# Kernel tuning notes

Hardware: AMD Instinct MI355X
Metric: run time of the kernel (lower is better)

## Reference

```python
import jax, jax.numpy as jnp
import numpy as np

N = 32767      # 2**15 - 1 nodes: complete binary tree, parent(i) = (i-1)//2
IN = 512       # in_channels
H = 256        # hidden_dim
OUT = 1        # output_dim
DEPTH = 15     # number of topological levels (static)


def setup_inputs() -> dict:
    key = jax.random.key(0)
    ks = jax.random.split(key, 8)
    x = jax.random.normal(ks[0], (N, IN), dtype=jnp.float32)
    # complete binary tree edge list: edge_index[0]=child, edge_index[1]=parent
    src = jnp.arange(1, N, dtype=jnp.int32)
    dst = (src - 1) // 2
    edge_index = jnp.stack([src, dst])  # [2, N-1]
    s = 1.0 / np.sqrt(H)  # torch LSTMCell/Linear default uniform init scale
    W_ih = jax.random.uniform(ks[1], (4 * H, IN), minval=-s, maxval=s, dtype=jnp.float32)
    W_hh = jax.random.uniform(ks[2], (4 * H, H), minval=-s, maxval=s, dtype=jnp.float32)
    b_ih = jax.random.uniform(ks[3], (4 * H,), minval=-s, maxval=s, dtype=jnp.float32)
    b_hh = jax.random.uniform(ks[4], (4 * H,), minval=-s, maxval=s, dtype=jnp.float32)
    W_fc = jax.random.uniform(ks[5], (OUT, H), minval=-s, maxval=s, dtype=jnp.float32)
    b_fc = jax.random.uniform(ks[6], (OUT,), minval=-s, maxval=s, dtype=jnp.float32)
    return {"x": x, "edge_index": edge_index, "W_ih": W_ih, "W_hh": W_hh,
            "b_ih": b_ih, "b_hh": b_hh, "W_fc": W_fc, "b_fc": b_fc}


def reference(x, edge_index, W_ih, W_hh, b_ih, b_hh, W_fc, b_fc):
    src, dst = edge_index[0], edge_index[1]
    # children count per parent (matches torch children_count loop)
    cnt = jax.ops.segment_sum(jnp.ones_like(src, dtype=x.dtype), dst, num_segments=N)
    cnt = jnp.maximum(cnt, 1.0)[:, None]  # [N,1]; leaves get zero child state anyway
    h = jnp.zeros((N, H), dtype=x.dtype)
    c = jnp.zeros((N, H), dtype=x.dtype)
    # topological sweep: deepest level first (children processed before parents)
    for d in range(DEPTH - 1, -1, -1):
        lo = 2 ** d - 1
        hi = min(2 ** (d + 1) - 1, N)  # level d node index range (static)
        # mean of already-computed child h/c states, gathered via edge list
        mean_h = jax.ops.segment_sum(h[src], dst, num_segments=N)[lo:hi] / cnt[lo:hi]
        mean_c = jax.ops.segment_sum(c[src], dst, num_segments=N)[lo:hi] / cnt[lo:hi]
        # torch LSTMCell: gates in (i, f, g, o) order
        gates = x[lo:hi] @ W_ih.T + b_ih + mean_h @ W_hh.T + b_hh  # [n_level, 4H]
        i, f, g, o = jnp.split(gates, 4, axis=-1)
        i, f, o = jax.nn.sigmoid(i), jax.nn.sigmoid(f), jax.nn.sigmoid(o)
        g = jnp.tanh(g)
        c_new = f * mean_c + i * g
        h_new = o * jnp.tanh(c_new)
        h = h.at[lo:hi].set(h_new)
        c = c.at[lo:hi].set(c_new)
    pooled = jnp.mean(h, axis=0, keepdims=True)  # [1, H]
    out = pooled @ W_fc.T + b_fc                 # [1, 1]
    return out.squeeze(-1)                       # [1]
```

## Files before the change

kernel.cpp:

```cpp
#include <hip/hip_runtime.h>
#include <math.h>


#define N_NODES 32767
#define N_LEAF0 16383
#define IN_C    512
#define H_C     256

typedef __bf16 bf16x8 __attribute__((ext_vector_type(8)));
typedef float  f32x4  __attribute__((ext_vector_type(4)));

__device__ __forceinline__ void gload_lds16(const void* g, void* l) {
    __builtin_amdgcn_global_load_lds(
        (const __attribute__((address_space(1))) unsigned int*)g,
        (__attribute__((address_space(3))) unsigned int*)l,
        16, 0, 0);
}

__device__ __forceinline__ float fast_rcp(float x) { return __builtin_amdgcn_rcpf(x); }
__device__ __forceinline__ float sigm(float x)     { return fast_rcp(1.f + __expf(-x)); }
__device__ __forceinline__ float tanh_fast(float x){ return 2.f * fast_rcp(1.f + __expf(-2.f * x)) - 1.f; }

__global__ __launch_bounds__(256)
void conv_bf16_kernel(const float* __restrict__ src, __bf16* __restrict__ dst, int n8)
{
    const int i = blockIdx.x * 256 + threadIdx.x;
    if (i < n8) {
        const float4* s4 = (const float4*)src;
        const float4 a = s4[2 * i];
        const float4 b = s4[2 * i + 1];
        bf16x8 o;
        o[0] = (__bf16)a.x; o[1] = (__bf16)a.y; o[2] = (__bf16)a.z; o[3] = (__bf16)a.w;
        o[4] = (__bf16)b.x; o[5] = (__bf16)b.y; o[6] = (__bf16)b.z; o[7] = (__bf16)b.w;
        *(bf16x8*)(dst + 8 * i) = o;
    }
}

__global__ __launch_bounds__(256)
void bulk_xw(const float* __restrict__ x,
             const __bf16* __restrict__ wih,
             const float* __restrict__ b_ih,
             const float* __restrict__ b_hh,
             __bf16* __restrict__ hb,
             float* __restrict__ c,
             __bf16* __restrict__ gx)
{
    __shared__ __bf16 As[128 * 32];
    __shared__ __bf16 Bs[128 * 32];

    const int t    = threadIdx.x;
    const int lane = t & 63;
    const int wv   = t >> 6;
    const int wm   = wv >> 1;
    const int wn   = wv & 1;
    const int quad = lane >> 4;
    const int l15  = lane & 15;
    const int cb   = blockIdx.x;
    const int m0   = blockIdx.y * 128;

    f32x4 acc[4][4];
#pragma unroll
    for (int mi = 0; mi < 4; ++mi)
#pragma unroll
        for (int ni = 0; ni < 4; ++ni) acc[mi][ni] = (f32x4)0.f;

    for (int k0 = 0; k0 < IN_C; k0 += 32) {
#pragma unroll
        for (int e = 0; e < 2; ++e) {
            const int chunk = wv * 2 + e;
            const int nl    = chunk * 16 + (lane >> 2);
            const int q     = (nl >> 4) & 3;
            const int cc    = (nl & 15) + ((nl >> 6) << 4);
            const int grow  = q * H_C + cb * 32 + cc;
            const void* g = (const char*)(wih + grow * IN_C + k0) + (lane & 3) * 16;
            gload_lds16(g, (char*)Bs + chunk * 1024);
        }
        {
            const int row  = t >> 1;
            const int kh   = (t & 1) * 16;
            const int node = min(m0 + row, N_NODES - 1);
            const float4* xs = (const float4*)(x + (size_t)node * IN_C + k0 + kh);
            const float4 v0 = xs[0], v1 = xs[1], v2 = xs[2], v3 = xs[3];
            bf16x8 o0, o1;
            o0[0] = (__bf16)v0.x; o0[1] = (__bf16)v0.y; o0[2] = (__bf16)v0.z; o0[3] = (__bf16)v0.w;
            o0[4] = (__bf16)v1.x; o0[5] = (__bf16)v1.y; o0[6] = (__bf16)v1.z; o0[7] = (__bf16)v1.w;
            o1[0] = (__bf16)v2.x; o1[1] = (__bf16)v2.y; o1[2] = (__bf16)v2.z; o1[3] = (__bf16)v2.w;
            o1[4] = (__bf16)v3.x; o1[5] = (__bf16)v3.y; o1[6] = (__bf16)v3.z; o1[7] = (__bf16)v3.w;
            bf16x8* dst = (bf16x8*)(As + row * 32 + kh);
            dst[0] = o0;
            dst[1] = o1;
        }
        __syncthreads();
        bf16x8 af[4], bfr[4];
#pragma unroll
        for (int mi = 0; mi < 4; ++mi)
            af[mi] = *(const bf16x8*)(As + (wm * 64 + mi * 16 + l15) * 32 + quad * 8);
#pragma unroll
        for (int ni = 0; ni < 4; ++ni)
            bfr[ni] = *(const bf16x8*)(Bs + (wn * 64 + ni * 16 + l15) * 32 + quad * 8);
#pragma unroll
        for (int mi = 0; mi < 4; ++mi)
#pragma unroll
            for (int ni = 0; ni < 4; ++ni)
                acc[mi][ni] = __builtin_amdgcn_mfma_f32_16x16x32_bf16(
                    af[mi], bfr[ni], acc[mi][ni], 0, 0, 0);
        __syncthreads();
    }

    const int CH = cb * 32 + wn * 16 + l15;
    float bs[4];
#pragma unroll
    for (int q = 0; q < 4; ++q) bs[q] = b_ih[q * H_C + CH] + b_hh[q * H_C + CH];

#pragma unroll
    for (int mi = 0; mi < 4; ++mi) {
#pragma unroll
        for (int r = 0; r < 4; ++r) {
            const int m = m0 + wm * 64 + mi * 16 + quad * 4 + r;
            if (m >= N_NODES) continue;
            if (m >= N_LEAF0) {
                const float gi = sigm(acc[mi][0][r] + bs[0]);
                const float gf = sigm(acc[mi][1][r] + bs[1]);  (void)gf;
                const float gg = tanh_fast(acc[mi][2][r] + bs[2]);
                const float go = sigm(acc[mi][3][r] + bs[3]);
                const float cn = gi * gg;
                const float hn = go * tanh_fast(cn);
                c[(size_t)m * H_C + CH] = cn;
                hb[(size_t)m * H_C + CH] = (__bf16)hn;
            } else {
#pragma unroll
                for (int q = 0; q < 4; ++q)
                    gx[(size_t)m * 1024 + q * H_C + CH] = (__bf16)acc[mi][q][r];
            }
        }
    }
}

__global__ __launch_bounds__(256)
void level_hw(const __bf16* __restrict__ whh,
              const float* __restrict__ b_ih,
              const float* __restrict__ b_hh,
              const __bf16* __restrict__ gx,
              __bf16* __restrict__ hb,
              float* __restrict__ c,
              int lo, int n)
{
    __shared__ __bf16 As[128 * 32];
    __shared__ __bf16 Bs[128 * 32];

    const int t    = threadIdx.x;
    const int lane = t & 63;
    const int wv   = t >> 6;
    const int wm   = wv >> 1;
    const int wn   = wv & 1;
    const int quad = lane >> 4;
    const int l15  = lane & 15;
    const int cb   = blockIdx.x;
    const int m0   = blockIdx.y * 128;

    f32x4 acc[4][4];
#pragma unroll
    for (int mi = 0; mi < 4; ++mi)
#pragma unroll
        for (int ni = 0; ni < 4; ++ni) acc[mi][ni] = (f32x4)0.f;

    for (int k0 = 0; k0 < H_C; k0 += 32) {
#pragma unroll
        for (int e = 0; e < 2; ++e) {
            const int chunk = wv * 2 + e;
            const int nl    = chunk * 16 + (lane >> 2);
            const int q     = (nl >> 4) & 3;
            const int cc    = (nl & 15) + ((nl >> 6) << 4);
            const int grow  = q * H_C + cb * 32 + cc;
            const void* g = (const char*)(whh + grow * H_C + k0) + (lane & 3) * 16;
            gload_lds16(g, (char*)Bs + chunk * 1024);
        }
        {
            const int row  = t >> 1;
            const int kh   = (t & 1) * 16;
            const int node = lo + m0 + row;
            const int k2   = k0 + kh;
            const bf16x8* hl = (const bf16x8*)(hb + (size_t)(2 * node + 1) * H_C + k2);
            const bf16x8* hr = (const bf16x8*)(hb + (size_t)(2 * node + 2) * H_C + k2);
            const bf16x8 a0 = hl[0], a1 = hl[1], b0 = hr[0], b1 = hr[1];
            bf16x8 o0, o1;
#pragma unroll
            for (int j = 0; j < 8; ++j) {
                o0[j] = (__bf16)(0.5f * ((float)a0[j] + (float)b0[j]));
                o1[j] = (__bf16)(0.5f * ((float)a1[j] + (float)b1[j]));
            }
            bf16x8* dst = (bf16x8*)(As + row * 32 + kh);
            dst[0] = o0;
            dst[1] = o1;
        }
        __syncthreads();
        bf16x8 af[4], bfr[4];
#pragma unroll
        for (int mi = 0; mi < 4; ++mi)
            af[mi] = *(const bf16x8*)(As + (wm * 64 + mi * 16 + l15) * 32 + quad * 8);
#pragma unroll
        for (int ni = 0; ni < 4; ++ni)
            bfr[ni] = *(const bf16x8*)(Bs + (wn * 64 + ni * 16 + l15) * 32 + quad * 8);
#pragma unroll
        for (int mi = 0; mi < 4; ++mi)
#pragma unroll
            for (int ni = 0; ni < 4; ++ni)
                acc[mi][ni] = __builtin_amdgcn_mfma_f32_16x16x32_bf16(
                    af[mi], bfr[ni], acc[mi][ni], 0, 0, 0);
        __syncthreads();
    }

    const int CH = cb * 32 + wn * 16 + l15;
    float bs[4];
#pragma unroll
    for (int q = 0; q < 4; ++q) bs[q] = b_ih[q * H_C + CH] + b_hh[q * H_C + CH];

#pragma unroll
    for (int mi = 0; mi < 4; ++mi) {
#pragma unroll
        for (int r = 0; r < 4; ++r) {
            const int m = m0 + wm * 64 + mi * 16 + quad * 4 + r;
            if (m < n) {
                const int node = lo + m;
                const float g0 = acc[mi][0][r] + (float)gx[(size_t)node * 1024 + 0 * H_C + CH] + bs[0];
                const float g1 = acc[mi][1][r] + (float)gx[(size_t)node * 1024 + 1 * H_C + CH] + bs[1];
                const float g2 = acc[mi][2][r] + (float)gx[(size_t)node * 1024 + 2 * H_C + CH] + bs[2];
                const float g3 = acc[mi][3][r] + (float)gx[(size_t)node * 1024 + 3 * H_C + CH] + bs[3];
                const float gi = sigm(g0);
                const float gf = sigm(g1);
                const float gg = tanh_fast(g2);
                const float go = sigm(g3);
                const float mc = 0.5f * (c[(size_t)(2 * node + 1) * H_C + CH] +
                                         c[(size_t)(2 * node + 2) * H_C + CH]);
                const float cn = gf * mc + gi * gg;
                const float hn = go * tanh_fast(cn);
                c[(size_t)node * H_C + CH] = cn;
                hb[(size_t)node * H_C + CH] = (__bf16)hn;
            }
        }
    }
}

__global__ __launch_bounds__(256)
void reduce_rows(const __bf16* __restrict__ hb, float* __restrict__ part)
{
    const int tcol = threadIdx.x;
    const int b = blockIdx.x;
    float s = 0.f;
    for (int r = 0; r < 128; ++r) {
        const int row = b * 128 + r;
        if (row < N_NODES) s += (float)hb[(size_t)row * H_C + tcol];
    }
    part[b * H_C + tcol] = s;
}

__global__ __launch_bounds__(256)
void reduce_final(const float* __restrict__ part,
                  const float* __restrict__ W_fc,
                  const float* __restrict__ b_fc,
                  float* __restrict__ out)
{
    __shared__ float sm[256];
    const int t = threadIdx.x;
    float s = 0.f;
    for (int j = 0; j < 256; ++j) s += part[j * H_C + t];
    s = s * (1.0f / (float)N_NODES) * W_fc[t];
    sm[t] = s;
    __syncthreads();
    for (int st = 128; st > 0; st >>= 1) {
        if (t < st) sm[t] += sm[t + st];
        __syncthreads();
    }
    if (t == 0) out[0] = sm[0] + b_fc[0];
}

extern "C" void kernel_launch(void* const* d_in, const int* in_sizes, int n_in,
                              void* d_out, int out_size, void* d_ws, size_t ws_size,
                              hipStream_t stream)
{
    const float* x    = (const float*)d_in[0];
    const float* W_ih = (const float*)d_in[2];
    const float* W_hh = (const float*)d_in[3];
    const float* b_ih = (const float*)d_in[4];
    const float* b_hh = (const float*)d_in[5];
    const float* W_fc = (const float*)d_in[6];
    const float* b_fc = (const float*)d_in[7];
    float* out = (float*)d_out;

    char* w = (char*)d_ws;
    __bf16* hb   = (__bf16*)w;  w += (size_t)N_NODES * H_C * 2;
    float*  c    = (float*)w;   w += (size_t)N_NODES * H_C * 4;
    __bf16* gx   = (__bf16*)w;  w += (size_t)N_LEAF0 * 1024 * 2;
    __bf16* wihb = (__bf16*)w;  w += (size_t)4 * H_C * IN_C * 2;
    __bf16* whhb = (__bf16*)w;  w += (size_t)4 * H_C * H_C * 2;
    float*  part = (float*)w;

    {
        const int n8i = (4 * H_C * IN_C) / 8;
        conv_bf16_kernel<<<(n8i + 255) / 256, 256, 0, stream>>>(W_ih, wihb, n8i);
        const int n8h = (4 * H_C * H_C) / 8;
        conv_bf16_kernel<<<(n8h + 255) / 256, 256, 0, stream>>>(W_hh, whhb, n8h);
    }

    {
        dim3 grid(8, 256);
        bulk_xw<<<grid, 256, 0, stream>>>(x, wihb, b_ih, b_hh, hb, c, gx);
    }
    for (int d = 13; d >= 0; --d) {
        const int n  = 1 << d;
        const int lo = n - 1;
        dim3 grid(8, (n + 127) / 128);
        level_hw<<<grid, 256, 0, stream>>>(whhb, b_ih, b_hh, gx, hb, c, lo, n);
    }
    reduce_rows<<<256, 256, 0, stream>>>(hb, part);
    reduce_final<<<1, 256, 0, stream>>>(part, W_fc, b_fc, out);
}
```

Baseline: 450.4 us.

## Fuse small tree levels into cooperative kernel, swizzle and deepen GEMM tiles

The last seven small levels of the tree now run in one cooperative kernel on 8 blocks. Each block keeps its slice of W_hh and the cell state in LDS and uses grid syncs between levels instead of separate launches. The bulk x·W_ih GEMM uses a K-step of 64 with XOR-swizzled LDS layouts and a 1D grid remapped for locality. level_hw gets the same block remap, and reduce_rows switches to vectorized bf16x8 loads. The intent is to remove launch overhead and tail latency on the serial small levels and to reduce LDS bank conflicts. The cost is a dependency on cooperative launch, which has a fallback path if the launch fails.

Result: faster. 422.1 us (-6.3%).

```diff
diff --git a/kernel.cpp b/kernel.cpp
--- a/kernel.cpp
+++ b/kernel.cpp
@@ -1,5 +1,8 @@
 #include <hip/hip_runtime.h>
+#include <hip/hip_cooperative_groups.h>
 #include <math.h>
+
+namespace cg = cooperative_groups;
 
 
 #define N_NODES 32767
@@ -45,8 +48,8 @@
              float* __restrict__ c,
              __bf16* __restrict__ gx)
 {
-    __shared__ __bf16 As[128 * 32];
-    __shared__ __bf16 Bs[128 * 32];
+    __shared__ __bf16 As[128 * 64];
+    __shared__ __bf16 Bs[128 * 64];
 
     const int t    = threadIdx.x;
     const int lane = t & 63;
@@ -55,8 +58,11 @@
     const int wn   = wv & 1;
     const int quad = lane >> 4;
     const int l15  = lane & 15;
-    const int cb   = blockIdx.x;
-    const int m0   = blockIdx.y * 128;
+
+    const int i  = blockIdx.x;
+    const int cb = (i >> 3) & 7;
+    const int mt = (i & 7) | ((i >> 6) << 3);
+    const int m0 = mt * 128;
 
     f32x4 acc[4][4];
 #pragma unroll
@@ -64,46 +70,54 @@
 #pragma unroll
         for (int ni = 0; ni < 4; ++ni) acc[mi][ni] = (f32x4)0.f;
 
-    for (int k0 = 0; k0 < IN_C; k0 += 32) {
-#pragma unroll
-        for (int e = 0; e < 2; ++e) {
-            const int chunk = wv * 2 + e;
-            const int nl    = chunk * 16 + (lane >> 2);
-            const int q     = (nl >> 4) & 3;
-            const int cc    = (nl & 15) + ((nl >> 6) << 4);
-            const int grow  = q * H_C + cb * 32 + cc;
-            const void* g = (const char*)(wih + grow * IN_C + k0) + (lane & 3) * 16;
-            gload_lds16(g, (char*)Bs + chunk * 1024);
+    for (int k0 = 0; k0 < IN_C; k0 += 64) {
+#pragma unroll
+        for (int e = 0; e < 4; ++e) {
+            const int ch = (wv * 4 + e) * 64 + lane;
+            const int nl = ch >> 3;
+            const int k8 = (ch & 7) ^ (nl & 7);
+            const int q  = (nl >> 4) & 3;
+            const int cc = (nl & 15) | ((nl >> 6) << 4);
+            const int grow = q * H_C + cb * 32 + cc;
+            gload_lds16(wih + (size_t)grow * IN_C + k0 + k8 * 8,
+                        (char*)Bs + (wv * 4 + e) * 1024);
         }
         {
             const int row  = t >> 1;
-            const int kh   = (t & 1) * 16;
+            const int kh   = (t & 1) * 32;
             const int node = min(m0 + row, N_NODES - 1);
             const float4* xs = (const float4*)(x + (size_t)node * IN_C + k0 + kh);
-            const float4 v0 = xs[0], v1 = xs[1], v2 = xs[2], v3 = xs[3];
-            bf16x8 o0, o1;
-            o0[0] = (__bf16)v0.x; o0[1] = (__bf16)v0.y; o0[2] = (__bf16)v0.z; o0[3] = (__bf16)v0.w;
-            o0[4] = (__bf16)v1.x; o0[5] = (__bf16)v1.y; o0[6] = (__bf16)v1.z; o0[7] = (__bf16)v1.w;
-            o1[0] = (__bf16)v2.x; o1[1] = (__bf16)v2.y; o1[2] = (__bf16)v2.z; o1[3] = (__bf16)v2.w;
-            o1[4] = (__bf16)v3.x; o1[5] = (__bf16)v3.y; o1[6] = (__bf16)v3.z; o1[7] = (__bf16)v3.w;
-            bf16x8* dst = (bf16x8*)(As + row * 32 + kh);
-            dst[0] = o0;
-            dst[1] = o1;
-        }
-        __syncthreads();
-        bf16x8 af[4], bfr[4];
-#pragma unroll
-        for (int mi = 0; mi < 4; ++mi)
-            af[mi] = *(const bf16x8*)(As + (wm * 64 + mi * 16 + l15) * 32 + quad * 8);
-#pragma unroll
-        for (int ni = 0; ni < 4; ++ni)
-            bfr[ni] = *(const bf16x8*)(Bs + (wn * 64 + ni * 16 + l15) * 32 + quad * 8);
-#pragma unroll
-        for (int mi = 0; mi < 4; ++mi)
-#pragma unroll
-            for (int ni = 0; ni < 4; ++ni)
-                acc[mi][ni] = __builtin_amdgcn_mfma_f32_16x16x32_bf16(
-                    af[mi], bfr[ni], acc[mi][ni], 0, 0, 0);
+#pragma unroll
+            for (int j = 0; j < 4; ++j) {
+                const float4 v0 = xs[2 * j], v1 = xs[2 * j + 1];
+                bf16x8 o;
+                o[0] = (__bf16)v0.x; o[1] = (__bf16)v0.y; o[2] = (__bf16)v0.z; o[3] = (__bf16)v0.w;
+                o[4] = (__bf16)v1.x; o[5] = (__bf16)v1.y; o[6] = (__bf16)v1.z; o[7] = (__bf16)v1.w;
+                const int cs = ((kh >> 3) + j) ^ (row & 7);
+                *(bf16x8*)(As + row * 64 + cs * 8) = o;
+            }
+        }
+        __syncthreads();
+#pragma unroll
+        for (int ks = 0; ks < 2; ++ks) {
+            bf16x8 af[4], bfr[4];
+#pragma unroll
+            for (int mi = 0; mi < 4; ++mi) {
+                const int row = wm * 64 + mi * 16 + l15;
+                af[mi] = *(const bf16x8*)(As + row * 64 + (((ks * 4 + quad) ^ (row & 7)) << 3));
+            }
+#pragma unroll
+            for (int ni = 0; ni < 4; ++ni) {
+                const int row = wn * 64 + ni * 16 + l15;
+                bfr[ni] = *(const bf16x8*)(Bs + row * 64 + (((ks * 4 + quad) ^ (row & 7)) << 3));
+            }
+#pragma unroll
+            for (int mi = 0; mi < 4; ++mi)
+#pragma unroll
+                for (int ni = 0; ni < 4; ++ni)
+                    acc[mi][ni] = __builtin_amdgcn_mfma_f32_16x16x32_bf16(
+                        af[mi], bfr[ni], acc[mi][ni], 0, 0, 0);
+        }
         __syncthreads();
     }
 
@@ -155,8 +169,12 @@
     const int wn   = wv & 1;
     const int quad = lane >> 4;
     const int l15  = lane & 15;
-    const int cb   = blockIdx.x;
-    const int m0   = blockIdx.y * 128;
+
+    const int i = blockIdx.x;
+    int cb, mt;
+    if (gridDim.x >= 64) { cb = (i >> 3) & 7; mt = (i & 7) | ((i >> 6) << 3); }
+    else                 { cb = i & 7;        mt = i >> 3; }
+    const int m0 = mt * 128;
 
     f32x4 acc[4][4];
 #pragma unroll
@@ -241,17 +259,144 @@
     }
 }
 
+__global__ __launch_bounds__(256, 1)
+void tail_levels(const __bf16* __restrict__ whh,
+                 const float* __restrict__ b_ih,
+                 const float* __restrict__ b_hh,
+                 const __bf16* __restrict__ gx,
+                 __bf16* __restrict__ hb,
+                 const float* __restrict__ c)
+{
+    __shared__ __bf16 Ws[128][264];
+    __shared__ __align__(16) char UAG[64 * 264 * 2];
+    __shared__ float cl[2][64][33];
+
+    const int t    = threadIdx.x;
+    const int cb   = blockIdx.x;
+    const int lane = t & 63;
+    const int wq   = t >> 6;
+    const int quad = lane >> 4;
+    const int l15  = lane & 15;
+
+    auto As = (__bf16(*)[264])UAG;
+    auto Gs = (float(*)[64][33])UAG;
+
+    {
+        const int row = t >> 1;
+        const int k0  = (t & 1) * 128;
+        const int q   = row >> 5, cc = row & 31;
+        const __bf16* src = whh + (size_t)(q * H_C + cb * 32 + cc) * H_C + k0;
+#pragma unroll
+        for (int j = 0; j < 16; ++j)
+            *(bf16x8*)(&Ws[row][k0 + 8 * j]) = *(const bf16x8*)(src + 8 * j);
+    }
+    const int ecc = t & 31;
+    const int erg = t >> 5;
+    const int CH  = cb * 32 + ecc;
+    float bsq[4];
+#pragma unroll
+    for (int q = 0; q < 4; ++q) bsq[q] = b_ih[q * H_C + CH] + b_hh[q * H_C + CH];
+
+    cg::grid_group grid = cg::this_grid();
+
+    for (int d = 6; d >= 0; --d) {
+        const int n  = 1 << d;
+        const int lo = n - 1;
+        const int pp = d & 1;
+        __syncthreads();
+        {
+            const int row  = t >> 2;
+            const int kb   = (t & 3) * 64;
+            const int node = lo + row;
+            const bf16x8* hl = (const bf16x8*)(hb + (size_t)(2 * node + 1) * H_C + kb);
+            const bf16x8* hr = (const bf16x8*)(hb + (size_t)(2 * node + 2) * H_C + kb);
+#pragma unroll
+            for (int j = 0; j < 8; ++j) {
+                const bf16x8 a = hl[j], b = hr[j];
+                bf16x8 o;
+#pragma unroll
+                for (int e = 0; e < 8; ++e)
+                    o[e] = (__bf16)(0.5f * ((float)a[e] + (float)b[e]));
+                *(bf16x8*)(&As[row][kb + 8 * j]) = o;
+            }
+        }
+        __syncthreads();
+        f32x4 acc[4][2];
+#pragma unroll
+        for (int mi = 0; mi < 4; ++mi)
+#pragma unroll
+            for (int ni = 0; ni < 2; ++ni) acc[mi][ni] = (f32x4)0.f;
+        for (int kk = 0; kk < 8; ++kk) {
+#pragma unroll
+            for (int mi = 0; mi < 4; ++mi) {
+                const bf16x8 af = *(const bf16x8*)(&As[mi * 16 + l15][kk * 32 + quad * 8]);
+#pragma unroll
+                for (int ni = 0; ni < 2; ++ni) {
+                    const bf16x8 bf_ = *(const bf16x8*)(&Ws[wq * 32 + ni * 16 + l15][kk * 32 + quad * 8]);
+                    acc[mi][ni] = __builtin_amdgcn_mfma_f32_16x16x32_bf16(af, bf_, acc[mi][ni], 0, 0, 0);
+                }
+            }
+        }
+        __syncthreads();
+#pragma unroll
+        for (int mi = 0; mi < 4; ++mi)
+#pragma unroll
+            for (int ni = 0; ni < 2; ++ni)
+#pragma unroll
+                for (int r = 0; r < 4; ++r)
+                    Gs[wq][mi * 16 + quad * 4 + r][ni * 16 + l15] = acc[mi][ni][r];
+        __syncthreads();
+        for (int r = erg; r < n; r += 8) {
+            const int node = lo + r;
+            float g[4];
+#pragma unroll
+            for (int q = 0; q < 4; ++q)
+                g[q] = Gs[q][r][ecc] + (float)gx[(size_t)node * 1024 + q * H_C + CH] + bsq[q];
+            const float gi = sigm(g[0]);
+            const float gf = sigm(g[1]);
+            const float gg = tanh_fast(g[2]);
+            const float go = sigm(g[3]);
+            float mc;
+            if (d == 6)
+                mc = 0.5f * (c[(size_t)(2 * node + 1) * H_C + CH] +
+                             c[(size_t)(2 * node + 2) * H_C + CH]);
+            else
+                mc = 0.5f * (cl[pp ^ 1][2 * r][ecc] + cl[pp ^ 1][2 * r + 1][ecc]);
+            const float cn = gf * mc + gi * gg;
+            const float hn = go * tanh_fast(cn);
+            cl[pp][r][ecc] = cn;
+            hb[(size_t)node * H_C + CH] = (__bf16)hn;
+        }
+        grid.sync();
+    }
+}
+
 __global__ __launch_bounds__(256)
 void reduce_rows(const __bf16* __restrict__ hb, float* __restrict__ part)
 {
-    const int tcol = threadIdx.x;
-    const int b = blockIdx.x;
-    float s = 0.f;
-    for (int r = 0; r < 128; ++r) {
-        const int row = b * 128 + r;
-        if (row < N_NODES) s += (float)hb[(size_t)row * H_C + tcol];
-    }
-    part[b * H_C + tcol] = s;
+    __shared__ float sm[8][256];
+    const int t  = threadIdx.x;
+    const int b  = blockIdx.x;
+    const int rg = t >> 5;
+    const int c8 = (t & 31) * 8;
+    float s[8];
+#pragma unroll
+    for (int j = 0; j < 8; ++j) s[j] = 0.f;
+    for (int i2 = 0; i2 < 16; ++i2) {
+        const int row = b * 128 + i2 * 8 + rg;
+        if (row < N_NODES) {
+            const bf16x8 v = *(const bf16x8*)(hb + (size_t)row * H_C + c8);
+#pragma unroll
+            for (int j = 0; j < 8; ++j) s[j] += (float)v[j];
+        }
+    }
+#pragma unroll
+    for (int j = 0; j < 8; ++j) sm[rg][c8 + j] = s[j];
+    __syncthreads();
+    float tot = 0.f;
+#pragma unroll
+    for (int g = 0; g < 8; ++g) tot += sm[g][t];
+    part[b * H_C + t] = tot;
 }
 
 __global__ __launch_bounds__(256)
@@ -302,16 +447,30 @@
         conv_bf16_kernel<<<(n8h + 255) / 256, 256, 0, stream>>>(W_hh, whhb, n8h);
     }
 
-    {
-        dim3 grid(8, 256);
-        bulk_xw<<<grid, 256, 0, stream>>>(x, wihb, b_ih, b_hh, hb, c, gx);
-    }
-    for (int d = 13; d >= 0; --d) {
+    bulk_xw<<<2048, 256, 0, stream>>>(x, wihb, b_ih, b_hh, hb, c, gx);
+
+    for (int d = 13; d >= 7; --d) {
         const int n  = 1 << d;
         const int lo = n - 1;
-        dim3 grid(8, (n + 127) / 128);
-        level_hw<<<grid, 256, 0, stream>>>(whhb, b_ih, b_hh, gx, hb, c, lo, n);
-    }
+        const int nm = (n + 127) / 128;
+        level_hw<<<nm * 8, 256, 0, stream>>>(whhb, b_ih, b_hh, gx, hb, c, lo, n);
+    }
+
+    {
+        const __bf16* a0 = whhb; const float* a1 = b_ih; const float* a2 = b_hh;
+        const __bf16* a3 = gx;   __bf16* a4 = hb;        const float* a5 = c;
+        void* targs[] = {&a0, &a1, &a2, &a3, &a4, &a5};
+        hipError_t e = hipLaunchCooperativeKernel((const void*)tail_levels,
+                                                  dim3(8), dim3(256), targs, 0, stream);
+        if (e != hipSuccess) {
+            for (int d = 6; d >= 0; --d) {
+                const int n  = 1 << d;
+                const int lo = n - 1;
+                level_hw<<<8, 256, 0, stream>>>(whhb, b_ih, b_hh, gx, hb, c, lo, n);
+            }
+        }
+    }
+
     reduce_rows<<<256, 256, 0, stream>>>(hb, part);
     reduce_final<<<1, 256, 0, stream>>>(part, W_fc, b_fc, out);
 }
```
